# Performance work log

Measured on AMD Instinct MI355X. Metric: run time of the kernel, lower is better.

## Reference

```python
import jax, jax.numpy as jnp
import numpy as np
from jax.scipy.special import ndtri

D = 1024
BITS = 4
K = 2 ** BITS
N = 4096


def _rotation_matrix(d, seed):
    # Haar-distributed random orthogonal matrix via QR with sign fix,
    # matching generate_rotation_matrix in the torch source.
    g = np.random.default_rng(seed).standard_normal((d, d)).astype(np.float32)
    Q, R = np.linalg.qr(g)
    s = np.sign(np.diag(R))
    s[s == 0] = 1.0
    return jnp.asarray((Q * s[None, :]).astype(np.float32))


def _lloyd_max_centroids(k):
    # Per-coordinate scalar codebook for a standard Gaussian (Lloyd-Max init
    # via inverse-CDF midpoints), analogous to LloydMaxCodebook.centroids [K].
    probs = (jnp.arange(k, dtype=jnp.float32) + 0.5) / k
    return ndtri(probs).astype(jnp.float32)


def setup_inputs() -> dict:
    key = jax.random.key(0)
    x = jax.random.normal(key, (N, D), dtype=jnp.float32)
    Pi = _rotation_matrix(D, seed=42)          # [d, d]
    centroids = _lloyd_max_centroids(K)        # [K]
    return {"x": x, "Pi": Pi, "centroids": centroids}


def reference(x, Pi, centroids):
    # rotate: y = x @ Pi^T
    y = x @ Pi.T                               # [N, d]
    # per-coordinate nearest-centroid argmin over K
    diffs = jnp.abs(y[..., None] - centroids)  # [N, d, K]
    indices = jnp.argmin(diffs, axis=-1)       # [N, d] int
    # dequantize: gather centroids, then unrotate x_hat = y_hat @ Pi
    y_hat = centroids[indices]                 # [N, d]
    x_hat = y_hat @ Pi                         # [N, d]
    return x_hat, indices
```

## Files before the change

kernel.cpp:

```cpp
#include <hip/hip_runtime.h>
#include <hip/hip_bf16.h>

#define TQ_D   1024
#define TQ_KC  16
#define MERGE_K 512
#define TQ_TOL  1.0e-4f
#define LCAP    1024

typedef __attribute__((ext_vector_type(8))) short bf16x8;
typedef __attribute__((ext_vector_type(8))) unsigned short ushort8;
typedef __attribute__((ext_vector_type(4))) float f32x4;

__device__ __forceinline__ unsigned short f2bf(float f) {
    union { __hip_bfloat16 h; unsigned short s; } u;
    u.h = __float2bfloat16(f);
    return u.s;
}
__device__ __forceinline__ float bf2f(unsigned short s) {
    union { unsigned int u; float f; } v;
    v.u = (unsigned int)s << 16;
    return v.f;
}

__global__ __launch_bounds__(256)
void tq_split(const float* __restrict__ In,
              unsigned short* __restrict__ Hi,
              unsigned short* __restrict__ Lo,
              int total4)
{
    for (int i = blockIdx.x * 256 + threadIdx.x; i < total4;
         i += gridDim.x * 256) {
        const float4 v = *((const float4*)In + i);
        ushort4 h, l;
        h.x = f2bf(v.x); l.x = f2bf(v.x - bf2f(h.x));
        h.y = f2bf(v.y); l.y = f2bf(v.y - bf2f(h.y));
        h.z = f2bf(v.z); l.z = f2bf(v.z - bf2f(h.z));
        h.w = f2bf(v.w); l.w = f2bf(v.w - bf2f(h.w));
        *((ushort4*)Hi + i) = h;
        *((ushort4*)Lo + i) = l;
    }
}

__global__ __launch_bounds__(512)
void tq_rq_mfma_pre(const unsigned short* __restrict__ Xh,
                    const unsigned short* __restrict__ Xl,
                    const unsigned short* __restrict__ Ph,
                    const unsigned short* __restrict__ Pl,
                    const float* __restrict__ Cent,
                    float* __restrict__ OutIdx,
                    unsigned short* __restrict__ Yh,
                    unsigned* __restrict__ Counter,
                    unsigned* __restrict__ List,
                    unsigned cap)
{
    __shared__ unsigned short XhS[128][40];
    __shared__ unsigned short XlS[128][40];
    __shared__ unsigned short PhS[64][40];
    __shared__ unsigned short PlS[64][40];
    __shared__ unsigned lcount;
    __shared__ unsigned gbase;
    __shared__ unsigned llist[LCAP];

    const int tid  = threadIdx.x;
    const int lane = tid & 63;
    const int wv   = tid >> 6;
    const int m0 = blockIdx.y * 128;
    const int n0 = blockIdx.x * 64;
    const int wr = (wv >> 1) * 32;
    const int wc = (wv & 1) * 32;
    const int l15 = lane & 15;
    const int k8  = (lane >> 4) * 8;

    const int srow = tid >> 2;
    const int scol = (tid & 3) * 8;
    const int brow = tid >> 3;
    const int bcol = (tid & 7) * 4;

    const unsigned short* aH = Xh + (size_t)(m0 + srow) * TQ_D + scol;
    const unsigned short* aL = Xl + (size_t)(m0 + srow) * TQ_D + scol;
    const unsigned short* bH = Ph + (size_t)(n0 + brow) * TQ_D + bcol;
    const unsigned short* bL = Pl + (size_t)(n0 + brow) * TQ_D + bcol;

    if (tid == 0) lcount = 0;

    f32x4 acc[2][2];
#pragma unroll
    for (int i = 0; i < 2; ++i)
#pragma unroll
        for (int j = 0; j < 2; ++j)
#pragma unroll
            for (int r = 0; r < 4; ++r) acc[i][j][r] = 0.0f;

    ushort8 vah, val;
    ushort4 vbh, vbl;
    vah = *(const ushort8*)(aH);
    val = *(const ushort8*)(aL);
    vbh = *(const ushort4*)(bH);
    vbl = *(const ushort4*)(bL);

    *(ushort8*)&XhS[srow][scol] = vah;
    *(ushort8*)&XlS[srow][scol] = val;
    *(ushort4*)&PhS[brow][bcol] = vbh;
    *(ushort4*)&PlS[brow][bcol] = vbl;
    __syncthreads();

    for (int kt = 0; kt < 32; ++kt) {
        const bool more = (kt + 1) < 32;
        if (more) {
            const int off = (kt + 1) * 32;
            vah = *(const ushort8*)(aH + off);
            val = *(const ushort8*)(aL + off);
            vbh = *(const ushort4*)(bH + off);
            vbl = *(const ushort4*)(bL + off);
        }

        bf16x8 afh[2], afl[2], bfh[2], bfl[2];
#pragma unroll
        for (int i = 0; i < 2; ++i) {
            afh[i] = *(const bf16x8*)&XhS[wr + i * 16 + l15][k8];
            afl[i] = *(const bf16x8*)&XlS[wr + i * 16 + l15][k8];
        }
#pragma unroll
        for (int j = 0; j < 2; ++j) {
            bfh[j] = *(const bf16x8*)&PhS[wc + j * 16 + l15][k8];
            bfl[j] = *(const bf16x8*)&PlS[wc + j * 16 + l15][k8];
        }

#pragma unroll
        for (int i = 0; i < 2; ++i)
#pragma unroll
            for (int j = 0; j < 2; ++j) {
                acc[i][j] = __builtin_amdgcn_mfma_f32_16x16x32_bf16(
                    afh[i], bfh[j], acc[i][j], 0, 0, 0);
                acc[i][j] = __builtin_amdgcn_mfma_f32_16x16x32_bf16(
                    afl[i], bfh[j], acc[i][j], 0, 0, 0);
                acc[i][j] = __builtin_amdgcn_mfma_f32_16x16x32_bf16(
                    afh[i], bfl[j], acc[i][j], 0, 0, 0);
                acc[i][j] = __builtin_amdgcn_mfma_f32_16x16x32_bf16(
                    afl[i], bfl[j], acc[i][j], 0, 0, 0);
            }

        if (more) {
            __syncthreads();
            *(ushort8*)&XhS[srow][scol] = vah;
            *(ushort8*)&XlS[srow][scol] = val;
            *(ushort4*)&PhS[brow][bcol] = vbh;
            *(ushort4*)&PlS[brow][bcol] = vbl;
            __syncthreads();
        }
    }

    float c[TQ_KC];
#pragma unroll
    for (int q = 0; q < TQ_KC; ++q) c[q] = Cent[q];

#pragma unroll
    for (int i = 0; i < 2; ++i)
#pragma unroll
        for (int j = 0; j < 2; ++j)
#pragma unroll
            for (int r = 0; r < 4; ++r) {
                const int row = m0 + wr + i * 16 + (lane >> 4) * 4 + r;
                const int col = n0 + wc + j * 16 + l15;
                const float y = acc[i][j][r];
                int best = 0;
                float bd = fabsf(y - c[0]);
#pragma unroll
                for (int q = 1; q < TQ_KC; ++q) {
                    const float d = fabsf(y - c[q]);
                    if (d < bd) { bd = d; best = q; }
                }
                float dist = 1e30f;
#pragma unroll
                for (int q = 0; q < TQ_KC - 1; ++q) {
                    const float mid = 0.5f * (c[q] + c[q + 1]);
                    dist = fminf(dist, fabsf(y - mid));
                }
                if (dist < TQ_TOL) {
                    const unsigned id = ((unsigned)row << 10) | (unsigned)col;
                    const unsigned ls = atomicAdd(&lcount, 1u);
                    if (ls < LCAP) {
                        llist[ls] = id;
                    } else {
                        const unsigned gs = atomicAdd(Counter, 1u);
                        if (gs < cap) List[gs] = id;
                    }
                }
                const size_t e = (size_t)row * TQ_D + col;
                OutIdx[e] = (float)best;
                Yh[e] = f2bf(c[best]);
            }

    __syncthreads();
    if (tid == 0) {
        const unsigned cnt = min(lcount, (unsigned)LCAP);
        gbase = (cnt > 0) ? atomicAdd(Counter, cnt) : 0u;
    }
    __syncthreads();
    const unsigned cnt = min(lcount, (unsigned)LCAP);
    for (unsigned s = tid; s < cnt; s += 512) {
        const unsigned g = gbase + s;
        if (g < cap) List[g] = llist[s];
    }
}

__global__ __launch_bounds__(512)
void tq_rq_mfma(const float* __restrict__ X,
                const float* __restrict__ Pi,
                const float* __restrict__ Cent,
                float* __restrict__ OutIdx,
                unsigned* __restrict__ Counter,
                unsigned* __restrict__ List,
                unsigned cap)
{
    __shared__ unsigned short XhS[128][40];
    __shared__ unsigned short XlS[128][40];
    __shared__ unsigned short PhS[64][40];
    __shared__ unsigned short PlS[64][40];
    __shared__ unsigned lcount;
    __shared__ unsigned gbase;
    __shared__ unsigned llist[LCAP];

    const int tid  = threadIdx.x;
    const int lane = tid & 63;
    const int wv   = tid >> 6;
    const int m0 = blockIdx.y * 128;
    const int n0 = blockIdx.x * 64;
    const int wr = (wv >> 1) * 32;
    const int wc = (wv & 1) * 32;
    const int l15 = lane & 15;
    const int k8  = (lane >> 4) * 8;

    const int srow = tid >> 2;
    const int scol = (tid & 3) * 8;
    const int brow = tid >> 3;
    const int bcol = (tid & 7) * 4;

    const float* aP = X  + (size_t)(m0 + srow) * TQ_D + scol;
    const float* bP = Pi + (size_t)(n0 + brow) * TQ_D + bcol;

    if (tid == 0) lcount = 0;

    f32x4 acc[2][2];
#pragma unroll
    for (int i = 0; i < 2; ++i)
#pragma unroll
        for (int j = 0; j < 2; ++j)
#pragma unroll
            for (int r = 0; r < 4; ++r) acc[i][j][r] = 0.0f;

    float4 va[2], vb;
#pragma unroll
    for (int q = 0; q < 2; ++q) va[q] = *(const float4*)(aP + 4 * q);
    vb = *(const float4*)(bP);

#pragma unroll
    for (int q = 0; q < 2; ++q) {
        ushort4 ah, al;
        const float* fa = (const float*)&va[q];
        ah.x = f2bf(fa[0]); al.x = f2bf(fa[0] - bf2f(ah.x));
        ah.y = f2bf(fa[1]); al.y = f2bf(fa[1] - bf2f(ah.y));
        ah.z = f2bf(fa[2]); al.z = f2bf(fa[2] - bf2f(ah.z));
        ah.w = f2bf(fa[3]); al.w = f2bf(fa[3] - bf2f(ah.w));
        *(ushort4*)&XhS[srow][scol + 4 * q] = ah;
        *(ushort4*)&XlS[srow][scol + 4 * q] = al;
    }
    {
        ushort4 bh, bl;
        const float* fb = (const float*)&vb;
        bh.x = f2bf(fb[0]); bl.x = f2bf(fb[0] - bf2f(bh.x));
        bh.y = f2bf(fb[1]); bl.y = f2bf(fb[1] - bf2f(bh.y));
        bh.z = f2bf(fb[2]); bl.z = f2bf(fb[2] - bf2f(bh.z));
        bh.w = f2bf(fb[3]); bl.w = f2bf(fb[3] - bf2f(bh.w));
        *(ushort4*)&PhS[brow][bcol] = bh;
        *(ushort4*)&PlS[brow][bcol] = bl;
    }
    __syncthreads();

    for (int kt = 0; kt < 32; ++kt) {
        const bool more = (kt + 1) < 32;
        if (more) {
            const float* ap = aP + (kt + 1) * 32;
            const float* bp = bP + (kt + 1) * 32;
#pragma unroll
            for (int q = 0; q < 2; ++q) va[q] = *(const float4*)(ap + 4 * q);
            vb = *(const float4*)(bp);
        }

        bf16x8 afh[2], afl[2], bfh[2], bfl[2];
#pragma unroll
        for (int i = 0; i < 2; ++i) {
            afh[i] = *(const bf16x8*)&XhS[wr + i * 16 + l15][k8];
            afl[i] = *(const bf16x8*)&XlS[wr + i * 16 + l15][k8];
        }
#pragma unroll
        for (int j = 0; j < 2; ++j) {
            bfh[j] = *(const bf16x8*)&PhS[wc + j * 16 + l15][k8];
            bfl[j] = *(const bf16x8*)&PlS[wc + j * 16 + l15][k8];
        }

#pragma unroll
        for (int i = 0; i < 2; ++i)
#pragma unroll
            for (int j = 0; j < 2; ++j) {
                acc[i][j] = __builtin_amdgcn_mfma_f32_16x16x32_bf16(
                    afh[i], bfh[j], acc[i][j], 0, 0, 0);
                acc[i][j] = __builtin_amdgcn_mfma_f32_16x16x32_bf16(
                    afl[i], bfh[j], acc[i][j], 0, 0, 0);
                acc[i][j] = __builtin_amdgcn_mfma_f32_16x16x32_bf16(
                    afh[i], bfl[j], acc[i][j], 0, 0, 0);
                acc[i][j] = __builtin_amdgcn_mfma_f32_16x16x32_bf16(
                    afl[i], bfl[j], acc[i][j], 0, 0, 0);
            }

        if (more) {
            __syncthreads();
#pragma unroll
            for (int q = 0; q < 2; ++q) {
                ushort4 ah, al;
                const float* fa = (const float*)&va[q];
                ah.x = f2bf(fa[0]); al.x = f2bf(fa[0] - bf2f(ah.x));
                ah.y = f2bf(fa[1]); al.y = f2bf(fa[1] - bf2f(ah.y));
                ah.z = f2bf(fa[2]); al.z = f2bf(fa[2] - bf2f(ah.z));
                ah.w = f2bf(fa[3]); al.w = f2bf(fa[3] - bf2f(ah.w));
                *(ushort4*)&XhS[srow][scol + 4 * q] = ah;
                *(ushort4*)&XlS[srow][scol + 4 * q] = al;
            }
            {
                ushort4 bh, bl;
                const float* fb = (const float*)&vb;
                bh.x = f2bf(fb[0]); bl.x = f2bf(fb[0] - bf2f(bh.x));
                bh.y = f2bf(fb[1]); bl.y = f2bf(fb[1] - bf2f(bh.y));
                bh.z = f2bf(fb[2]); bl.z = f2bf(fb[2] - bf2f(bh.z));
                bh.w = f2bf(fb[3]); bl.w = f2bf(fb[3] - bf2f(bh.w));
                *(ushort4*)&PhS[brow][bcol] = bh;
                *(ushort4*)&PlS[brow][bcol] = bl;
            }
            __syncthreads();
        }
    }

    float c[TQ_KC];
#pragma unroll
    for (int q = 0; q < TQ_KC; ++q) c[q] = Cent[q];

#pragma unroll
    for (int i = 0; i < 2; ++i)
#pragma unroll
        for (int j = 0; j < 2; ++j)
#pragma unroll
            for (int r = 0; r < 4; ++r) {
                const int row = m0 + wr + i * 16 + (lane >> 4) * 4 + r;
                const int col = n0 + wc + j * 16 + l15;
                const float y = acc[i][j][r];
                int best = 0;
                float bd = fabsf(y - c[0]);
#pragma unroll
                for (int q = 1; q < TQ_KC; ++q) {
                    const float d = fabsf(y - c[q]);
                    if (d < bd) { bd = d; best = q; }
                }
                float dist = 1e30f;
#pragma unroll
                for (int q = 0; q < TQ_KC - 1; ++q) {
                    const float mid = 0.5f * (c[q] + c[q + 1]);
                    dist = fminf(dist, fabsf(y - mid));
                }
                if (dist < TQ_TOL) {
                    const unsigned id = ((unsigned)row << 10) | (unsigned)col;
                    const unsigned ls = atomicAdd(&lcount, 1u);
                    if (ls < LCAP) {
                        llist[ls] = id;
                    } else {
                        const unsigned gs = atomicAdd(Counter, 1u);
                        if (gs < cap) List[gs] = id;
                    }
                }
                OutIdx[(size_t)row * TQ_D + col] = (float)best;
            }

    __syncthreads();
    if (tid == 0) {
        const unsigned cnt = min(lcount, (unsigned)LCAP);
        gbase = (cnt > 0) ? atomicAdd(Counter, cnt) : 0u;
    }
    __syncthreads();
    const unsigned cnt = min(lcount, (unsigned)LCAP);
    for (unsigned s = tid; s < cnt; s += 512) {
        const unsigned g = gbase + s;
        if (g < cap) List[g] = llist[s];
    }
}

__global__ __launch_bounds__(256)
void tq_fixup_lds(const float* __restrict__ X,
                  const float* __restrict__ Pi,
                  const float* __restrict__ Cent,
                  float* __restrict__ OutIdx,
                  unsigned short* __restrict__ Yh,
                  const unsigned* __restrict__ Counter,
                  const unsigned* __restrict__ List,
                  unsigned cap)
{
    __shared__ float Rows[8][2][1024];
    __shared__ float part[8][2];
    __shared__ unsigned ids[8];

    const int tid = threadIdx.x;
    const unsigned count = min(*Counter, cap);

    for (unsigned base = blockIdx.x * 8; base < count; base += gridDim.x * 8) {
        const unsigned nsus = min(8u, count - base);

        if (tid < 8) ids[tid] = (tid < nsus) ? List[base + tid] : 0u;
        __syncthreads();

#pragma unroll
        for (int q = 0; q < 16; ++q) {
            const int lin = q * 256 + tid;
            const int sus = lin >> 9;
            const int rowsel = (lin >> 8) & 1;
            const int f4 = lin & 255;
            if ((unsigned)sus < nsus) {
                const unsigned id = ids[sus];
                const int m = id >> 10;
                const int n = id & (TQ_D - 1);
                const float* src = rowsel ? (Pi + (size_t)n * TQ_D)
                                          : (X + (size_t)m * TQ_D);
                *(float4*)&Rows[sus][rowsel][f4 * 4] =
                    *(const float4*)(src + f4 * 4);
            }
        }
        __syncthreads();

        if (tid < 16 && (unsigned)(tid >> 1) < nsus) {
            const int sus = tid >> 1;
            const int p = tid & 1;
            const int kb = p * MERGE_K;
            float a = 0.0f;
            for (int k = 0; k < MERGE_K; k += 4) {
                const float4 xa = *(const float4*)&Rows[sus][0][kb + k];
                const float4 pa = *(const float4*)&Rows[sus][1][kb + k];
                a = fmaf(xa.x, pa.x, a);
                a = fmaf(xa.y, pa.y, a);
                a = fmaf(xa.z, pa.z, a);
                a = fmaf(xa.w, pa.w, a);
            }
            part[sus][p] = a;
        }
        __syncthreads();

        if (tid < (int)nsus) {
            const float y = part[tid][0] + part[tid][1];
            float c[TQ_KC];
#pragma unroll
            for (int q = 0; q < TQ_KC; ++q) c[q] = Cent[q];
            int best = 0;
            float bd = fabsf(y - c[0]);
#pragma unroll
            for (int q = 1; q < TQ_KC; ++q) {
                const float d = fabsf(y - c[q]);
                if (d < bd) { bd = d; best = q; }
            }
            const unsigned id = ids[tid];
            const size_t e = (size_t)(id >> 10) * TQ_D + (id & (TQ_D - 1));
            OutIdx[e] = (float)best;
            if (Yh) Yh[e] = f2bf(c[best]);
        }
        __syncthreads();
    }
}

__global__ __launch_bounds__(512)
void tq_dq_mfma_pre(const unsigned short* __restrict__ Yh,
                    const unsigned short* __restrict__ Ph,
                    float* __restrict__ Xhat)
{
    __shared__ unsigned short Ys[128][40];
    __shared__ unsigned short Ps[64][40];

    const int tid  = threadIdx.x;
    const int lane = tid & 63;
    const int wv   = tid >> 6;
    const int m0 = blockIdx.y * 128;
    const int n0 = blockIdx.x * 64;
    const int wr = (wv >> 1) * 32;
    const int wc = (wv & 1) * 32;
    const int l15 = lane & 15;
    const int k8  = (lane >> 4) * 8;

    const int srow = tid >> 2;
    const int scol = (tid & 3) * 8;
    const int bk = tid >> 4;
    const int bnq = (tid & 15) * 4;

    const unsigned short* aP = Yh + (size_t)(m0 + srow) * TQ_D + scol;
    const unsigned short* bP = Ph + (size_t)bk * TQ_D + n0 + bnq;

    f32x4 acc[2][2];
#pragma unroll
    for (int i = 0; i < 2; ++i)
#pragma unroll
        for (int j = 0; j < 2; ++j)
#pragma unroll
            for (int r = 0; r < 4; ++r) acc[i][j][r] = 0.0f;

    ushort8 va = *(const ushort8*)(aP);
    ushort4 vb = *(const ushort4*)(bP);

    *(ushort8*)&Ys[srow][scol] = va;
    Ps[bnq + 0][bk] = vb.x;
    Ps[bnq + 1][bk] = vb.y;
    Ps[bnq + 2][bk] = vb.z;
    Ps[bnq + 3][bk] = vb.w;
    __syncthreads();

    for (int kt = 0; kt < 32; ++kt) {
        const bool more = (kt + 1) < 32;
        if (more) {
            va = *(const ushort8*)(aP + (kt + 1) * 32);
            vb = *(const ushort4*)(bP + (size_t)(kt + 1) * 32 * TQ_D);
        }

        bf16x8 af[2], bfr[2];
#pragma unroll
        for (int i = 0; i < 2; ++i)
            af[i] = *(const bf16x8*)&Ys[wr + i * 16 + l15][k8];
#pragma unroll
        for (int j = 0; j < 2; ++j)
            bfr[j] = *(const bf16x8*)&Ps[wc + j * 16 + l15][k8];

#pragma unroll
        for (int i = 0; i < 2; ++i)
#pragma unroll
            for (int j = 0; j < 2; ++j)
                acc[i][j] = __builtin_amdgcn_mfma_f32_16x16x32_bf16(
                    af[i], bfr[j], acc[i][j], 0, 0, 0);

        if (more) {
            __syncthreads();
            *(ushort8*)&Ys[srow][scol] = va;
            Ps[bnq + 0][bk] = vb.x;
            Ps[bnq + 1][bk] = vb.y;
            Ps[bnq + 2][bk] = vb.z;
            Ps[bnq + 3][bk] = vb.w;
            __syncthreads();
        }
    }

#pragma unroll
    for (int i = 0; i < 2; ++i)
#pragma unroll
        for (int j = 0; j < 2; ++j)
#pragma unroll
            for (int r = 0; r < 4; ++r) {
                const int row = wr + i * 16 + (lane >> 4) * 4 + r;
                const int col = wc + j * 16 + l15;
                Xhat[(size_t)(m0 + row) * TQ_D + n0 + col] = acc[i][j][r];
            }
}

__global__ __launch_bounds__(512)
void tq_dq_mfma(const float* __restrict__ IdxF,
                const float* __restrict__ Pi,
                const float* __restrict__ Cent,
                float* __restrict__ Xhat)
{
    __shared__ unsigned short Ys[128][40];
    __shared__ unsigned short Ps[64][40];
    __shared__ unsigned short csb[TQ_KC];

    const int tid  = threadIdx.x;
    const int lane = tid & 63;
    const int wv   = tid >> 6;
    const int m0 = blockIdx.y * 128;
    const int n0 = blockIdx.x * 64;
    const int wr = (wv >> 1) * 32;
    const int wc = (wv & 1) * 32;
    const int l15 = lane & 15;
    const int k8  = (lane >> 4) * 8;

    const int srow = tid >> 2;
    const int scol = (tid & 3) * 8;
    const int bk = tid >> 4;
    const int bnq = (tid & 15) * 4;

    const float* aP = IdxF + (size_t)(m0 + srow) * TQ_D + scol;
    const float* bP = Pi + (size_t)bk * TQ_D + n0 + bnq;

    if (tid < TQ_KC) csb[tid] = f2bf(Cent[tid]);

    f32x4 acc[2][2];
#pragma unroll
    for (int i = 0; i < 2; ++i)
#pragma unroll
        for (int j = 0; j < 2; ++j)
#pragma unroll
            for (int r = 0; r < 4; ++r) acc[i][j][r] = 0.0f;

    float4 va[2], vb;
#pragma unroll
    for (int q = 0; q < 2; ++q) va[q] = *(const float4*)(aP + 4 * q);
    vb = *(const float4*)(bP);

    __syncthreads();

#pragma unroll
    for (int q = 0; q < 2; ++q) {
        ushort4 w;
        const float* fa = (const float*)&va[q];
        w.x = csb[(int)fa[0] & 15];
        w.y = csb[(int)fa[1] & 15];
        w.z = csb[(int)fa[2] & 15];
        w.w = csb[(int)fa[3] & 15];
        *(ushort4*)&Ys[srow][scol + 4 * q] = w;
    }
    {
        const float* fb = (const float*)&vb;
        Ps[bnq + 0][bk] = f2bf(fb[0]);
        Ps[bnq + 1][bk] = f2bf(fb[1]);
        Ps[bnq + 2][bk] = f2bf(fb[2]);
        Ps[bnq + 3][bk] = f2bf(fb[3]);
    }
    __syncthreads();

    for (int kt = 0; kt < 32; ++kt) {
        const bool more = (kt + 1) < 32;
        if (more) {
            const float* ap = aP + (kt + 1) * 32;
            const float* bp = bP + (size_t)(kt + 1) * 32 * TQ_D;
#pragma unroll
            for (int q = 0; q < 2; ++q) va[q] = *(const float4*)(ap + 4 * q);
            vb = *(const float4*)(bp);
        }

        bf16x8 af[2], bfr[2];
#pragma unroll
        for (int i = 0; i < 2; ++i)
            af[i] = *(const bf16x8*)&Ys[wr + i * 16 + l15][k8];
#pragma unroll
        for (int j = 0; j < 2; ++j)
            bfr[j] = *(const bf16x8*)&Ps[wc + j * 16 + l15][k8];

#pragma unroll
        for (int i = 0; i < 2; ++i)
#pragma unroll
            for (int j = 0; j < 2; ++j)
                acc[i][j] = __builtin_amdgcn_mfma_f32_16x16x32_bf16(
                    af[i], bfr[j], acc[i][j], 0, 0, 0);

        if (more) {
            __syncthreads();
#pragma unroll
            for (int q = 0; q < 2; ++q) {
                ushort4 w;
                const float* fa = (const float*)&va[q];
                w.x = csb[(int)fa[0] & 15];
                w.y = csb[(int)fa[1] & 15];
                w.z = csb[(int)fa[2] & 15];
                w.w = csb[(int)fa[3] & 15];
                *(ushort4*)&Ys[srow][scol + 4 * q] = w;
            }
            {
                const float* fb = (const float*)&vb;
                Ps[bnq + 0][bk] = f2bf(fb[0]);
                Ps[bnq + 1][bk] = f2bf(fb[1]);
                Ps[bnq + 2][bk] = f2bf(fb[2]);
                Ps[bnq + 3][bk] = f2bf(fb[3]);
            }
            __syncthreads();
        }
    }

#pragma unroll
    for (int i = 0; i < 2; ++i)
#pragma unroll
        for (int j = 0; j < 2; ++j)
#pragma unroll
            for (int r = 0; r < 4; ++r) {
                const int row = wr + i * 16 + (lane >> 4) * 4 + r;
                const int col = wc + j * 16 + l15;
                Xhat[(size_t)(m0 + row) * TQ_D + n0 + col] = acc[i][j][r];
            }
}

extern "C" void kernel_launch(void* const* d_in, const int* in_sizes, int n_in,
                              void* d_out, int out_size, void* d_ws, size_t ws_size,
                              hipStream_t stream)
{
    const float* x    = (const float*)d_in[0];
    const float* Pi   = (const float*)d_in[1];
    const float* cent = (const float*)d_in[2];
    float* out = (float*)d_out;

    const int ND = in_sizes[0];
    const int DD = in_sizes[1];
    const int N  = ND / TQ_D;

    float* xhat = out;
    float* oidx = out + ND;

    unsigned* counter = (unsigned*)xhat;
    unsigned* list    = (unsigned*)xhat + 16;
    const unsigned cap = (unsigned)(ND - 16);

    hipMemsetAsync(counter, 0, 4, stream);

    dim3 grid1(TQ_D / 64, N / 128);

    const size_t wsNeed = 2ull * (3ull * ND + 2ull * DD);
    if (ws_size >= wsNeed) {
        unsigned short* Xh = (unsigned short*)d_ws;
        unsigned short* Xl = Xh + ND;
        unsigned short* Ph = Xl + ND;
        unsigned short* Pl = Ph + DD;
        unsigned short* Yh = Pl + DD;

        tq_split<<<2048, 256, 0, stream>>>(x, Xh, Xl, ND / 4);
        tq_split<<<1024, 256, 0, stream>>>(Pi, Ph, Pl, DD / 4);
        tq_rq_mfma_pre<<<grid1, 512, 0, stream>>>(Xh, Xl, Ph, Pl, cent, oidx,
                                                  Yh, counter, list, cap);
        tq_fixup_lds<<<1024, 256, 0, stream>>>(x, Pi, cent, oidx, Yh,
                                               counter, list, cap);
        tq_dq_mfma_pre<<<grid1, 512, 0, stream>>>(Yh, Ph, xhat);
    } else {
        tq_rq_mfma<<<grid1, 512, 0, stream>>>(x, Pi, cent, oidx,
                                              counter, list, cap);
        tq_fixup_lds<<<1024, 256, 0, stream>>>(x, Pi, cent, oidx, nullptr,
                                               counter, list, cap);
        tq_dq_mfma<<<grid1, 512, 0, stream>>>(oidx, Pi, cent, xhat);
    }
}
```

Baseline: 112.4 us.

## Load MFMA operands directly from global memory and pre-transpose Pi for dequant

Both GEMM kernels on the workspace path drop LDS staging and the per-k-step barriers, so each wave reads its bf16 MFMA fragments straight from global memory and relies on L1/L2 for reuse. A new transpose kernel writes a transposed bf16 copy of Pi's high part, which lets the dequant GEMM read B fragments contiguously along K. The aim is to remove LDS traffic and synchronization stalls. In exchange, operand reuse across waves now depends on the cache, fragment loads are strided row reads, there is no software prefetch, and the transpose adds an extra launch.

After: 214.0 us. 90.5% more time.

```diff
diff --git a/kernel.cpp b/kernel.cpp
--- a/kernel.cpp
+++ b/kernel.cpp
@@ -41,22 +41,41 @@
     }
 }
 
+__global__ __launch_bounds__(256)
+void tq_transpose(const unsigned short* __restrict__ S,
+                  unsigned short* __restrict__ T)
+{
+    __shared__ unsigned short tile[64][68];
+    const int tid = threadIdx.x;
+    const int k0 = blockIdx.y * 64;
+    const int n0 = blockIdx.x * 64;
+#pragma unroll
+    for (int q = 0; q < 16; ++q) {
+        const int idx = q * 256 + tid;
+        const int r = idx >> 6, c = idx & 63;
+        tile[r][c] = S[(size_t)(k0 + r) * TQ_D + n0 + c];
+    }
+    __syncthreads();
+#pragma unroll
+    for (int q = 0; q < 16; ++q) {
+        const int idx = q * 256 + tid;
+        const int r = idx >> 6, c = idx & 63;
+        T[(size_t)(n0 + r) * TQ_D + k0 + c] = tile[c][r];
+    }
+}
+
 __global__ __launch_bounds__(512)
-void tq_rq_mfma_pre(const unsigned short* __restrict__ Xh,
-                    const unsigned short* __restrict__ Xl,
-                    const unsigned short* __restrict__ Ph,
-                    const unsigned short* __restrict__ Pl,
-                    const float* __restrict__ Cent,
-                    float* __restrict__ OutIdx,
-                    unsigned short* __restrict__ Yh,
-                    unsigned* __restrict__ Counter,
-                    unsigned* __restrict__ List,
-                    unsigned cap)
-{
-    __shared__ unsigned short XhS[128][40];
-    __shared__ unsigned short XlS[128][40];
-    __shared__ unsigned short PhS[64][40];
-    __shared__ unsigned short PlS[64][40];
+void tq_rq_mfma_gd(const unsigned short* __restrict__ Xh,
+                   const unsigned short* __restrict__ Xl,
+                   const unsigned short* __restrict__ Ph,
+                   const unsigned short* __restrict__ Pl,
+                   const float* __restrict__ Cent,
+                   float* __restrict__ OutIdx,
+                   unsigned short* __restrict__ Yh,
+                   unsigned* __restrict__ Counter,
+                   unsigned* __restrict__ List,
+                   unsigned cap)
+{
     __shared__ unsigned lcount;
     __shared__ unsigned gbase;
     __shared__ unsigned llist[LCAP];
@@ -71,17 +90,15 @@
     const int l15 = lane & 15;
     const int k8  = (lane >> 4) * 8;
 
-    const int srow = tid >> 2;
-    const int scol = (tid & 3) * 8;
-    const int brow = tid >> 3;
-    const int bcol = (tid & 7) * 4;
-
-    const unsigned short* aH = Xh + (size_t)(m0 + srow) * TQ_D + scol;
-    const unsigned short* aL = Xl + (size_t)(m0 + srow) * TQ_D + scol;
-    const unsigned short* bH = Ph + (size_t)(n0 + brow) * TQ_D + bcol;
-    const unsigned short* bL = Pl + (size_t)(n0 + brow) * TQ_D + bcol;
-
     if (tid == 0) lcount = 0;
+    __syncthreads();
+
+    const size_t arow = (size_t)(m0 + wr + l15) * TQ_D + k8;
+    const size_t brow = (size_t)(n0 + wc + l15) * TQ_D + k8;
+    const unsigned short* aH = Xh + arow;
+    const unsigned short* aL = Xl + arow;
+    const unsigned short* bH = Ph + brow;
+    const unsigned short* bL = Pl + brow;
 
     f32x4 acc[2][2];
 #pragma unroll
@@ -91,39 +108,18 @@
 #pragma unroll
             for (int r = 0; r < 4; ++r) acc[i][j][r] = 0.0f;
 
-    ushort8 vah, val;
-    ushort4 vbh, vbl;
-    vah = *(const ushort8*)(aH);
-    val = *(const ushort8*)(aL);
-    vbh = *(const ushort4*)(bH);
-    vbl = *(const ushort4*)(bL);
-
-    *(ushort8*)&XhS[srow][scol] = vah;
-    *(ushort8*)&XlS[srow][scol] = val;
-    *(ushort4*)&PhS[brow][bcol] = vbh;
-    *(ushort4*)&PlS[brow][bcol] = vbl;
-    __syncthreads();
-
     for (int kt = 0; kt < 32; ++kt) {
-        const bool more = (kt + 1) < 32;
-        if (more) {
-            const int off = (kt + 1) * 32;
-            vah = *(const ushort8*)(aH + off);
-            val = *(const ushort8*)(aL + off);
-            vbh = *(const ushort4*)(bH + off);
-            vbl = *(const ushort4*)(bL + off);
-        }
-
+        const int off = kt * 32;
         bf16x8 afh[2], afl[2], bfh[2], bfl[2];
 #pragma unroll
         for (int i = 0; i < 2; ++i) {
-            afh[i] = *(const bf16x8*)&XhS[wr + i * 16 + l15][k8];
-            afl[i] = *(const bf16x8*)&XlS[wr + i * 16 + l15][k8];
+            afh[i] = *(const bf16x8*)(aH + (size_t)i * 16 * TQ_D + off);
+            afl[i] = *(const bf16x8*)(aL + (size_t)i * 16 * TQ_D + off);
         }
 #pragma unroll
         for (int j = 0; j < 2; ++j) {
-            bfh[j] = *(const bf16x8*)&PhS[wc + j * 16 + l15][k8];
-            bfl[j] = *(const bf16x8*)&PlS[wc + j * 16 + l15][k8];
+            bfh[j] = *(const bf16x8*)(bH + (size_t)j * 16 * TQ_D + off);
+            bfl[j] = *(const bf16x8*)(bL + (size_t)j * 16 * TQ_D + off);
         }
 
 #pragma unroll
@@ -139,15 +135,6 @@
                 acc[i][j] = __builtin_amdgcn_mfma_f32_16x16x32_bf16(
                     afl[i], bfl[j], acc[i][j], 0, 0, 0);
             }
-
-        if (more) {
-            __syncthreads();
-            *(ushort8*)&XhS[srow][scol] = vah;
-            *(ushort8*)&XlS[srow][scol] = val;
-            *(ushort4*)&PhS[brow][bcol] = vbh;
-            *(ushort4*)&PlS[brow][bcol] = vbl;
-            __syncthreads();
-        }
     }
 
     float c[TQ_KC];
@@ -205,6 +192,141 @@
 }
 
 __global__ __launch_bounds__(512)
+void tq_dq_mfma_gd(const unsigned short* __restrict__ Yh,
+                   const unsigned short* __restrict__ PhT,
+                   float* __restrict__ Xhat)
+{
+    const int tid  = threadIdx.x;
+    const int lane = tid & 63;
+    const int wv   = tid >> 6;
+    const int m0 = blockIdx.y * 128;
+    const int n0 = blockIdx.x * 64;
+    const int wr = (wv >> 1) * 32;
+    const int wc = (wv & 1) * 32;
+    const int l15 = lane & 15;
+    const int k8  = (lane >> 4) * 8;
+
+    const unsigned short* aP = Yh  + (size_t)(m0 + wr + l15) * TQ_D + k8;
+    const unsigned short* bP = PhT + (size_t)(n0 + wc + l15) * TQ_D + k8;
+
+    f32x4 acc[2][2];
+#pragma unroll
+    for (int i = 0; i < 2; ++i)
+#pragma unroll
+        for (int j = 0; j < 2; ++j)
+#pragma unroll
+            for (int r = 0; r < 4; ++r) acc[i][j][r] = 0.0f;
+
+    for (int kt = 0; kt < 32; ++kt) {
+        const int off = kt * 32;
+        bf16x8 af[2], bfr[2];
+#pragma unroll
+        for (int i = 0; i < 2; ++i)
+            af[i] = *(const bf16x8*)(aP + (size_t)i * 16 * TQ_D + off);
+#pragma unroll
+        for (int j = 0; j < 2; ++j)
+            bfr[j] = *(const bf16x8*)(bP + (size_t)j * 16 * TQ_D + off);
+
+#pragma unroll
+        for (int i = 0; i < 2; ++i)
+#pragma unroll
+            for (int j = 0; j < 2; ++j)
+                acc[i][j] = __builtin_amdgcn_mfma_f32_16x16x32_bf16(
+                    af[i], bfr[j], acc[i][j], 0, 0, 0);
+    }
+
+#pragma unroll
+    for (int i = 0; i < 2; ++i)
+#pragma unroll
+        for (int j = 0; j < 2; ++j)
+#pragma unroll
+            for (int r = 0; r < 4; ++r) {
+                const int row = m0 + wr + i * 16 + (lane >> 4) * 4 + r;
+                const int col = n0 + wc + j * 16 + l15;
+                Xhat[(size_t)row * TQ_D + col] = acc[i][j][r];
+            }
+}
+
+__global__ __launch_bounds__(256)
+void tq_fixup_lds(const float* __restrict__ X,
+                  const float* __restrict__ Pi,
+                  const float* __restrict__ Cent,
+                  float* __restrict__ OutIdx,
+                  unsigned short* __restrict__ Yh,
+                  const unsigned* __restrict__ Counter,
+                  const unsigned* __restrict__ List,
+                  unsigned cap)
+{
+    __shared__ float Rows[8][2][1024];
+    __shared__ float part[8][2];
+    __shared__ unsigned ids[8];
+
+    const int tid = threadIdx.x;
+    const unsigned count = min(*Counter, cap);
+
+    for (unsigned base = blockIdx.x * 8; base < count; base += gridDim.x * 8) {
+        const unsigned nsus = min(8u, count - base);
+
+        if (tid < 8) ids[tid] = (tid < nsus) ? List[base + tid] : 0u;
+        __syncthreads();
+
+#pragma unroll
+        for (int q = 0; q < 16; ++q) {
+            const int lin = q * 256 + tid;
+            const int sus = lin >> 9;
+            const int rowsel = (lin >> 8) & 1;
+            const int f4 = lin & 255;
+            if ((unsigned)sus < nsus) {
+                const unsigned id = ids[sus];
+                const int m = id >> 10;
+                const int n = id & (TQ_D - 1);
+                const float* src = rowsel ? (Pi + (size_t)n * TQ_D)
+                                          : (X + (size_t)m * TQ_D);
+                *(float4*)&Rows[sus][rowsel][f4 * 4] =
+                    *(const float4*)(src + f4 * 4);
+            }
+        }
+        __syncthreads();
+
+        if (tid < 16 && (unsigned)(tid >> 1) < nsus) {
+            const int sus = tid >> 1;
+            const int p = tid & 1;
+            const int kb = p * MERGE_K;
+            float a = 0.0f;
+            for (int k = 0; k < MERGE_K; k += 4) {
+                const float4 xa = *(const float4*)&Rows[sus][0][kb + k];
+                const float4 pa = *(const float4*)&Rows[sus][1][kb + k];
+                a = fmaf(xa.x, pa.x, a);
+                a = fmaf(xa.y, pa.y, a);
+                a = fmaf(xa.z, pa.z, a);
+                a = fmaf(xa.w, pa.w, a);
+            }
+            part[sus][p] = a;
+        }
+        __syncthreads();
+
+        if (tid < (int)nsus) {
+            const float y = part[tid][0] + part[tid][1];
+            float c[TQ_KC];
+#pragma unroll
+            for (int q = 0; q < TQ_KC; ++q) c[q] = Cent[q];
+            int best = 0;
+            float bd = fabsf(y - c[0]);
+#pragma unroll
+            for (int q = 1; q < TQ_KC; ++q) {
+                const float d = fabsf(y - c[q]);
+                if (d < bd) { bd = d; best = q; }
+            }
+            const unsigned id = ids[tid];
+            const size_t e = (size_t)(id >> 10) * TQ_D + (id & (TQ_D - 1));
+            OutIdx[e] = (float)best;
+            if (Yh) Yh[e] = f2bf(c[best]);
+        }
+        __syncthreads();
+    }
+}
+
+__global__ __launch_bounds__(512)
 void tq_rq_mfma(const float* __restrict__ X,
                 const float* __restrict__ Pi,
                 const float* __restrict__ Cent,
@@ -392,92 +514,15 @@
     }
 }
 
-__global__ __launch_bounds__(256)
-void tq_fixup_lds(const float* __restrict__ X,
-                  const float* __restrict__ Pi,
-                  const float* __restrict__ Cent,
-                  float* __restrict__ OutIdx,
-                  unsigned short* __restrict__ Yh,
-                  const unsigned* __restrict__ Counter,
-                  const unsigned* __restrict__ List,
-                  unsigned cap)
-{
-    __shared__ float Rows[8][2][1024];
-    __shared__ float part[8][2];
-    __shared__ unsigned ids[8];
-
-    const int tid = threadIdx.x;
-    const unsigned count = min(*Counter, cap);
-
-    for (unsigned base = blockIdx.x * 8; base < count; base += gridDim.x * 8) {
-        const unsigned nsus = min(8u, count - base);
-
-        if (tid < 8) ids[tid] = (tid < nsus) ? List[base + tid] : 0u;
-        __syncthreads();
-
-#pragma unroll
-        for (int q = 0; q < 16; ++q) {
-            const int lin = q * 256 + tid;
-            const int sus = lin >> 9;
-            const int rowsel = (lin >> 8) & 1;
-            const int f4 = lin & 255;
-            if ((unsigned)sus < nsus) {
-                const unsigned id = ids[sus];
-                const int m = id >> 10;
-                const int n = id & (TQ_D - 1);
-                const float* src = rowsel ? (Pi + (size_t)n * TQ_D)
-                                          : (X + (size_t)m * TQ_D);
-                *(float4*)&Rows[sus][rowsel][f4 * 4] =
-                    *(const float4*)(src + f4 * 4);
-            }
-        }
-        __syncthreads();
-
-        if (tid < 16 && (unsigned)(tid >> 1) < nsus) {
-            const int sus = tid >> 1;
-            const int p = tid & 1;
-            const int kb = p * MERGE_K;
-            float a = 0.0f;
-            for (int k = 0; k < MERGE_K; k += 4) {
-                const float4 xa = *(const float4*)&Rows[sus][0][kb + k];
-                const float4 pa = *(const float4*)&Rows[sus][1][kb + k];
-                a = fmaf(xa.x, pa.x, a);
-                a = fmaf(xa.y, pa.y, a);
-                a = fmaf(xa.z, pa.z, a);
-                a = fmaf(xa.w, pa.w, a);
-            }
-            part[sus][p] = a;
-        }
-        __syncthreads();
-
-        if (tid < (int)nsus) {
-            const float y = part[tid][0] + part[tid][1];
-            float c[TQ_KC];
-#pragma unroll
-            for (int q = 0; q < TQ_KC; ++q) c[q] = Cent[q];
-            int best = 0;
-            float bd = fabsf(y - c[0]);
-#pragma unroll
-            for (int q = 1; q < TQ_KC; ++q) {
-                const float d = fabsf(y - c[q]);
-                if (d < bd) { bd = d; best = q; }
-            }
-            const unsigned id = ids[tid];
-            const size_t e = (size_t)(id >> 10) * TQ_D + (id & (TQ_D - 1));
-            OutIdx[e] = (float)best;
-            if (Yh) Yh[e] = f2bf(c[best]);
-        }
-        __syncthreads();
-    }
-}
-
 __global__ __launch_bounds__(512)
-void tq_dq_mfma_pre(const unsigned short* __restrict__ Yh,
-                    const unsigned short* __restrict__ Ph,
-                    float* __restrict__ Xhat)
+void tq_dq_mfma(const float* __restrict__ IdxF,
+                const float* __restrict__ Pi,
+                const float* __restrict__ Cent,
+                float* __restrict__ Xhat)
 {
     __shared__ unsigned short Ys[128][40];
     __shared__ unsigned short Ps[64][40];
+    __shared__ unsigned short csb[TQ_KC];
 
     const int tid  = threadIdx.x;
     const int lane = tid & 63;
@@ -494,97 +539,6 @@
     const int bk = tid >> 4;
     const int bnq = (tid & 15) * 4;
 
-    const unsigned short* aP = Yh + (size_t)(m0 + srow) * TQ_D + scol;
-    const unsigned short* bP = Ph + (size_t)bk * TQ_D + n0 + bnq;
-
-    f32x4 acc[2][2];
-#pragma unroll
-    for (int i = 0; i < 2; ++i)
-#pragma unroll
-        for (int j = 0; j < 2; ++j)
-#pragma unroll
-            for (int r = 0; r < 4; ++r) acc[i][j][r] = 0.0f;
-
-    ushort8 va = *(const ushort8*)(aP);
-    ushort4 vb = *(const ushort4*)(bP);
-
-    *(ushort8*)&Ys[srow][scol] = va;
-    Ps[bnq + 0][bk] = vb.x;
-    Ps[bnq + 1][bk] = vb.y;
-    Ps[bnq + 2][bk] = vb.z;
-    Ps[bnq + 3][bk] = vb.w;
-    __syncthreads();
-
-    for (int kt = 0; kt < 32; ++kt) {
-        const bool more = (kt + 1) < 32;
-        if (more) {
-            va = *(const ushort8*)(aP + (kt + 1) * 32);
-            vb = *(const ushort4*)(bP + (size_t)(kt + 1) * 32 * TQ_D);
-        }
-
-        bf16x8 af[2], bfr[2];
-#pragma unroll
-        for (int i = 0; i < 2; ++i)
-            af[i] = *(const bf16x8*)&Ys[wr + i * 16 + l15][k8];
-#pragma unroll
-        for (int j = 0; j < 2; ++j)
-            bfr[j] = *(const bf16x8*)&Ps[wc + j * 16 + l15][k8];
-
-#pragma unroll
-        for (int i = 0; i < 2; ++i)
-#pragma unroll
-            for (int j = 0; j < 2; ++j)
-                acc[i][j] = __builtin_amdgcn_mfma_f32_16x16x32_bf16(
-                    af[i], bfr[j], acc[i][j], 0, 0, 0);
-
-        if (more) {
-            __syncthreads();
-            *(ushort8*)&Ys[srow][scol] = va;
-            Ps[bnq + 0][bk] = vb.x;
-            Ps[bnq + 1][bk] = vb.y;
-            Ps[bnq + 2][bk] = vb.z;
-            Ps[bnq + 3][bk] = vb.w;
-            __syncthreads();
-        }
-    }
-
-#pragma unroll
-    for (int i = 0; i < 2; ++i)
-#pragma unroll
-        for (int j = 0; j < 2; ++j)
-#pragma unroll
-            for (int r = 0; r < 4; ++r) {
-                const int row = wr + i * 16 + (lane >> 4) * 4 + r;
-                const int col = wc + j * 16 + l15;
-                Xhat[(size_t)(m0 + row) * TQ_D + n0 + col] = acc[i][j][r];
-            }
-}
-
-__global__ __launch_bounds__(512)
-void tq_dq_mfma(const float* __restrict__ IdxF,
-                const float* __restrict__ Pi,
-                const float* __restrict__ Cent,
-                float* __restrict__ Xhat)
-{
-    __shared__ unsigned short Ys[128][40];
-    __shared__ unsigned short Ps[64][40];
-    __shared__ unsigned short csb[TQ_KC];
-
-    const int tid  = threadIdx.x;
-    const int lane = tid & 63;
-    const int wv   = tid >> 6;
-    const int m0 = blockIdx.y * 128;
-    const int n0 = blockIdx.x * 64;
-    const int wr = (wv >> 1) * 32;
-    const int wc = (wv & 1) * 32;
-    const int l15 = lane & 15;
-    const int k8  = (lane >> 4) * 8;
-
-    const int srow = tid >> 2;
-    const int scol = (tid & 3) * 8;
-    const int bk = tid >> 4;
-    const int bnq = (tid & 15) * 4;
-
     const float* aP = IdxF + (size_t)(m0 + srow) * TQ_D + scol;
     const float* bP = Pi + (size_t)bk * TQ_D + n0 + bnq;
 
@@ -708,21 +662,25 @@
 
     dim3 grid1(TQ_D / 64, N / 128);
 
-    const size_t wsNeed = 2ull * (3ull * ND + 2ull * DD);
+    const size_t wsNeed = 2ull * (3ull * ND + 3ull * DD);
     if (ws_size >= wsNeed) {
-        unsigned short* Xh = (unsigned short*)d_ws;
-        unsigned short* Xl = Xh + ND;
-        unsigned short* Ph = Xl + ND;
-        unsigned short* Pl = Ph + DD;
-        unsigned short* Yh = Pl + DD;
+        unsigned short* Xh  = (unsigned short*)d_ws;
+        unsigned short* Xl  = Xh + ND;
+        unsigned short* Ph  = Xl + ND;
+        unsigned short* Pl  = Ph + DD;
+        unsigned short* PhT = Pl + DD;
+        unsigned short* Yh  = PhT + DD;
 
         tq_split<<<2048, 256, 0, stream>>>(x, Xh, Xl, ND / 4);
         tq_split<<<1024, 256, 0, stream>>>(Pi, Ph, Pl, DD / 4);
-        tq_rq_mfma_pre<<<grid1, 512, 0, stream>>>(Xh, Xl, Ph, Pl, cent, oidx,
-                                                  Yh, counter, list, cap);
+        dim3 gridT(TQ_D / 64, TQ_D / 64);
+        tq_transpose<<<gridT, 256, 0, stream>>>(Ph, PhT);
+
+        tq_rq_mfma_gd<<<grid1, 512, 0, stream>>>(Xh, Xl, Ph, Pl, cent, oidx,
+                                                 Yh, counter, list, cap);
         tq_fixup_lds<<<1024, 256, 0, stream>>>(x, Pi, cent, oidx, Yh,
                                                counter, list, cap);
-        tq_dq_mfma_pre<<<grid1, 512, 0, stream>>>(Yh, Ph, xhat);
+        tq_dq_mfma_gd<<<grid1, 512, 0, stream>>>(Yh, PhT, xhat);
     } else {
         tq_rq_mfma<<<grid1, 512, 0, stream>>>(x, Pi, cent, oidx,
                                               counter, list, cap);
```
